# Kernel tuning notes

Hardware: AMD Instinct MI355X
Metric: run time of the kernel (lower is better)

Reference implementation:

```python
import jax, jax.numpy as jnp
import numpy as np
import math

B, S, D, H = 4, 2048, 768, 12
HD = D // H  # 64


def setup_inputs() -> dict:
    key = jax.random.key(0)
    ks = jax.random.split(key, 9)
    s = 0.02
    return {
        "hidden_states": jax.random.normal(ks[0], (B, S, D), jnp.float32),
        "layout_q": jax.random.normal(ks[1], (B, S, D), jnp.float32),
        "layout_k": jax.random.normal(ks[2], (B, S, D), jnp.float32),
        "attention_mask": jnp.zeros((B, 1, 1, S), jnp.float32),
        "Wq": jax.random.normal(ks[3], (D, D), jnp.float32) * s,
        "bq": jnp.zeros((D,), jnp.float32),
        "Wk": jax.random.normal(ks[4], (D, D), jnp.float32) * s,
        "bk": jnp.zeros((D,), jnp.float32),
        "Wv": jax.random.normal(ks[5], (D, D), jnp.float32) * s,
        "bv": jnp.zeros((D,), jnp.float32),
    }


def _split_heads(x):
    # [B,S,D] -> [B,H,S,HD]
    return x.reshape(B, S, H, HD).transpose(0, 2, 1, 3)


def reference(hidden_states, layout_q, layout_k, attention_mask, Wq, bq, Wk, bk, Wv, bv):
    q = _split_heads(hidden_states @ Wq.T + bq)
    k = _split_heads(hidden_states @ Wk.T + bk)
    v = _split_heads(hidden_states @ Wv.T + bv)
    lq = _split_heads(layout_q)
    lk = _split_heads(layout_k)
    scale = 1.0 / math.sqrt(HD)
    # dual-stream scores: content + layout, both [B,H,S,S]
    scores = (jnp.einsum("bhqd,bhkd->bhqk", q, k)
              + jnp.einsum("bhqd,bhkd->bhqk", lq, lk)) * scale
    scores = scores + attention_mask
    probs = jax.nn.softmax(scores, axis=-1)
    ctx = jnp.einsum("bhqk,bhkd->bhqd", probs, v)
    return ctx.transpose(0, 2, 1, 3).reshape(B, S, D)
```

## Files before the change

### kernel.cpp

```cpp
#include <hip/hip_runtime.h>


typedef __attribute__((ext_vector_type(8))) short short8;
typedef __attribute__((ext_vector_type(4))) float floatx4;

#define LOG2E 1.4426950408889634f
#define QSCL 0.18033688011112042f

static constexpr int Sn = 2048, Dn = 768, Hn = 12, BHn = 48;

__device__ __forceinline__ unsigned short f2bf(float f) {
  unsigned u = __float_as_uint(f);
  u += 0x7FFFu + ((u >> 16) & 1u);
  return (unsigned short)(u >> 16);
}

typedef const __attribute__((address_space(1))) unsigned int* gas_t;
typedef __attribute__((address_space(3))) unsigned int* las_t;
__device__ __forceinline__ void async16(const void* g, void* l) {
  __builtin_amdgcn_global_load_lds((gas_t)g, (las_t)l, 16, 0, 0);
}

__global__ void cast_hs_kernel(const float* __restrict__ in, unsigned short* __restrict__ out, int n4) {
  int i = blockIdx.x * 256 + threadIdx.x;
  if (i >= n4) return;
  float4 v = ((const float4*)in)[i];
  ushort4 o = make_ushort4(f2bf(v.x), f2bf(v.y), f2bf(v.z), f2bf(v.w));
  ((ushort4*)out)[i] = o;
}

__global__ void cast_w_kernel(const float* __restrict__ w0, const float* __restrict__ w1,
                              const float* __restrict__ w2, unsigned short* __restrict__ out) {
  int i = blockIdx.x * 256 + threadIdx.x;
  const float* src = (blockIdx.y == 0) ? w0 : (blockIdx.y == 1) ? w1 : w2;
  float4 v = ((const float4*)src)[i];
  ushort4 o = make_ushort4(f2bf(v.x), f2bf(v.y), f2bf(v.z), f2bf(v.w));
  ((ushort4*)(out + (size_t)blockIdx.y * Dn * Dn))[i] = o;
}

__global__ void pack_layout_kernel(const float* __restrict__ lq, const float* __restrict__ lk,
                                   unsigned short* __restrict__ Qc, unsigned short* __restrict__ Kc) {
  int idx = blockIdx.x * 256 + threadIdx.x;
  const float* src = blockIdx.y ? lk : lq;
  unsigned short* dst = blockIdx.y ? Kc : Qc;
  const float sc = blockIdx.y ? 1.0f : QSCL;
  int d8 = idx & 7;
  int tt = idx >> 3;
  int h = tt % Hn;
  int bs = tt / Hn;
  int b = bs >> 11, s = bs & (Sn - 1);
  float4 v0 = ((const float4*)src)[idx * 2];
  float4 v1 = ((const float4*)src)[idx * 2 + 1];
  short8 o;
  o[0] = (short)f2bf(v0.x * sc); o[1] = (short)f2bf(v0.y * sc);
  o[2] = (short)f2bf(v0.z * sc); o[3] = (short)f2bf(v0.w * sc);
  o[4] = (short)f2bf(v1.x * sc); o[5] = (short)f2bf(v1.y * sc);
  o[6] = (short)f2bf(v1.z * sc); o[7] = (short)f2bf(v1.w * sc);
  size_t off = ((size_t)(b * Hn + h) * Sn + s) * 128 + 64 + d8 * 8;
  *(short8*)(dst + off) = o;
}

__global__ __launch_bounds__(256, 3)
void proj_kernel(const unsigned short* __restrict__ X,
                 const unsigned short* __restrict__ Wb,
                 const float* __restrict__ bq, const float* __restrict__ bk, const float* __restrict__ bv,
                 unsigned short* __restrict__ Qc, unsigned short* __restrict__ Kc,
                 unsigned short* __restrict__ Vt) {
  __shared__ __align__(16) unsigned short sMem[16384];
  unsigned short* const sA = sMem;
  unsigned short* const sB = sMem + 8192;

  const int z = blockIdx.z;
  const unsigned short* W = Wb + (size_t)z * Dn * Dn;
  const float* bias = (z == 0) ? bq : (z == 1) ? bk : bv;

  const int t = threadIdx.x;
  const int lane = t & 63, wave = t >> 6;
  const int wm = wave >> 1, wn = wave & 1;
  const int quad = lane >> 4, col15 = lane & 15;
  const int m0 = blockIdx.y * 128, n0 = blockIdx.x * 128;

  const int srow = lane >> 3, schunk = lane & 7;

  floatx4 acc[4][4];
#pragma unroll
  for (int i = 0; i < 4; i++)
#pragma unroll
    for (int j = 0; j < 4; j++) acc[i][j] = (floatx4){0.f, 0.f, 0.f, 0.f};

  for (int k0 = 0; k0 < Dn; k0 += 64) {
    __syncthreads();
#pragma unroll
    for (int c = 0; c < 4; c++) {
      int row = wave * 32 + c * 8 + srow;
      int g = schunk ^ (row & 7);
      async16(X + (size_t)(m0 + row) * Dn + k0 + g * 8, sA + (wave * 32 + c * 8) * 64);
      async16(W + (size_t)(n0 + row) * Dn + k0 + g * 8, sB + (wave * 32 + c * 8) * 64);
    }
    __syncthreads();
#pragma unroll
    for (int kk = 0; kk < 2; kk++) {
      short8 af[4], bf[4];
      const int slot = ((kk * 4 + quad) ^ (col15 & 7)) * 8;
#pragma unroll
      for (int i = 0; i < 4; i++)
        af[i] = *(const short8*)(sA + (wm * 64 + i * 16 + col15) * 64 + slot);
#pragma unroll
      for (int j = 0; j < 4; j++)
        bf[j] = *(const short8*)(sB + (wn * 64 + j * 16 + col15) * 64 + slot);
#pragma unroll
      for (int i = 0; i < 4; i++)
#pragma unroll
        for (int j = 0; j < 4; j++)
          acc[i][j] = __builtin_amdgcn_mfma_f32_16x16x32_bf16(af[i], bf[j], acc[i][j], 0, 0, 0);
    }
  }

  __syncthreads();
  const int b = m0 >> 11;
  const int s0g = m0 & (Sn - 1);
  const int h0 = n0 >> 6;

  if (z < 2) {
    const float scl = (z == 0) ? QSCL : 1.0f;
    unsigned short* dst0 = (z == 0) ? Qc : Kc;
#pragma unroll
    for (int j = 0; j < 4; j++) {
      int nl = wn * 64 + j * 16 + col15;
      float bias_n = bias[n0 + nl];
#pragma unroll
      for (int i = 0; i < 4; i++) {
        int mb = wm * 64 + i * 16 + quad * 4;
#pragma unroll
        for (int r = 0; r < 4; r++) {
          int m = mb + r;
          sMem[m * 128 + (nl ^ (((m >> 2) & 3) << 4))] = f2bf((acc[i][j][r] + bias_n) * scl);
        }
      }
    }
    __syncthreads();
#pragma unroll
    for (int cc = 0; cc < 8; cc++) {
      int idx = cc * 256 + t;
      int m = idx >> 4, piece = idx & 15;
      int h = h0 + (piece >> 3), d8 = piece & 7;
      short8 v = *(const short8*)(sMem + m * 128 + (piece ^ (((m >> 2) & 3) << 1)) * 8);
      *(short8*)(dst0 + ((size_t)(b * Hn + h) * Sn + s0g + m) * 128 + d8 * 8) = v;
    }
  } else {
#pragma unroll
    for (int j = 0; j < 4; j++) {
      int nl = wn * 64 + j * 16 + col15;
      float bias_n = bias[n0 + nl];
#pragma unroll
      for (int i = 0; i < 4; i++) {
        int mb = wm * 64 + i * 16 + quad * 4;
        ushort4 pk = make_ushort4(f2bf(acc[i][j][0] + bias_n), f2bf(acc[i][j][1] + bias_n),
                                  f2bf(acc[i][j][2] + bias_n), f2bf(acc[i][j][3] + bias_n));
        *(ushort4*)(sMem + nl * 128 + (mb ^ ((nl & 7) << 4))) = pk;
      }
    }
    __syncthreads();
#pragma unroll
    for (int cc = 0; cc < 8; cc++) {
      int idx = cc * 256 + t;
      int nl = idx >> 4, piece = idx & 15;
      int h = h0 + (nl >> 6), d = nl & 63;
      short8 v = *(const short8*)(sMem + nl * 128 + (piece ^ ((nl & 7) << 1)) * 8);
      *(short8*)(Vt + ((size_t)(b * Hn + h) * 64 + d) * Sn + s0g + piece * 8) = v;
    }
  }
}

__global__ __launch_bounds__(256, 2)
void attn_kernel(const unsigned short* __restrict__ Qc,
                 const unsigned short* __restrict__ Kc,
                 const unsigned short* __restrict__ Vt,
                 const float* __restrict__ mask,
                 float* __restrict__ out) {
  __shared__ __align__(16) unsigned short sK2[2][64 * 128];
  __shared__ __align__(16) unsigned short sV2[2][64 * 64];
  __shared__ __align__(16) unsigned short sS[128 * 64];

  const int t = threadIdx.x;
  const int lane = t & 63, wave = t >> 6;
  const int quad = lane >> 4, col15 = lane & 15;
  const int swz = (col15 & 7) << 3;

  const int id = blockIdx.x;
  const int slot = id >> 3;
  const int bh = (id & 7) + 8 * (slot >> 4);
  const int q0 = (slot & 15) * 128;
  const int b = bh / Hn, h = bh % Hn;

  short8 aq[2][4];
  const unsigned short* Qbase = Qc + ((size_t)bh * Sn + q0) * 128;
#pragma unroll
  for (int i = 0; i < 2; i++)
#pragma unroll
    for (int kk = 0; kk < 4; kk++)
      aq[i][kk] = *(const short8*)(Qbase + (size_t)(wave * 32 + i * 16 + col15) * 128 + kk * 32 + quad * 8);

  floatx4 O[2][4], lacc[2];
#pragma unroll
  for (int i = 0; i < 2; i++) {
    lacc[i] = (floatx4){0.f, 0.f, 0.f, 0.f};
#pragma unroll
    for (int j = 0; j < 4; j++) O[i][j] = (floatx4){0.f, 0.f, 0.f, 0.f};
  }

  short8 aone;
  {
    short onev = (col15 == 0) ? (short)0x3F80 : (short)0;
#pragma unroll
    for (int e = 0; e < 8; e++) aone[e] = onev;
  }

  const unsigned short* Kbase = Kc + (size_t)bh * Sn * 128;
  const unsigned short* Vbase = Vt + (size_t)bh * 64 * Sn;
  const float* mbase = mask + (size_t)b * Sn;

  const int krow = lane >> 4, kslot = lane & 15;
  const int vrow = lane >> 3, vslot = lane & 7;

  auto stageKV = [&](int tile, int buf) {
    unsigned short* sKn = &sK2[buf][0];
    unsigned short* sVn = &sV2[buf][0];
#pragma unroll
    for (int c = 0; c < 4; c++) {
      int row = wave * 16 + c * 4 + krow;
      int g = (kslot & 8) | ((kslot ^ row) & 7);
      async16(Kbase + (size_t)(tile * 64 + row) * 128 + g * 8, sKn + (wave * 16 + c * 4) * 128);
    }
#pragma unroll
    for (int c = 0; c < 2; c++) {
      int row = wave * 16 + c * 8 + vrow;
      int g = vslot ^ (row & 7);
      async16(Vbase + (size_t)row * Sn + tile * 64 + g * 8, sVn + (wave * 16 + c * 8) * 64);
    }
  };

  constexpr int NT = Sn / 64;
  stageKV(0, 0);
  float mcur = mbase[lane] * LOG2E;
  __syncthreads();

  for (int kt = 0; kt < NT; kt++) {
    const int cur = kt & 1;
    if (kt + 1 < NT) stageKV(kt + 1, cur ^ 1);
    const int tn = (kt + 1 < NT) ? kt + 1 : NT - 1;
    float mnew = mbase[tn * 64 + lane] * LOG2E;
    const bool nomask = __all(mcur == 0.0f);
    const unsigned short* sKcur = &sK2[cur][0];
    const unsigned short* sVcur = &sV2[cur][0];

    floatx4 sacc[4][2];
#pragma unroll
    for (int jm = 0; jm < 4; jm++) {
      sacc[jm][0] = (floatx4){0.f, 0.f, 0.f, 0.f};
      sacc[jm][1] = (floatx4){0.f, 0.f, 0.f, 0.f};
    }
    __builtin_amdgcn_s_setprio(1);
#pragma unroll
    for (int kk = 0; kk < 4; kk++) {
      const int slotK = (((kk * 4 + quad) & 8) | (((kk * 4 + quad) ^ col15) & 7)) * 8;
#pragma unroll
      for (int jm = 0; jm < 4; jm++) {
        short8 ak = *(const short8*)(sKcur + (jm * 16 + col15) * 128 + slotK);
        sacc[jm][0] = __builtin_amdgcn_mfma_f32_16x16x32_bf16(ak, aq[0][kk], sacc[jm][0], 0, 0, 0);
        sacc[jm][1] = __builtin_amdgcn_mfma_f32_16x16x32_bf16(ak, aq[1][kk], sacc[jm][1], 0, 0, 0);
      }
    }
    __builtin_amdgcn_s_setprio(0);

    float mvv[4][4];
    if (!nomask) {
#pragma unroll
      for (int jm = 0; jm < 4; jm++)
#pragma unroll
        for (int r = 0; r < 4; r++) mvv[jm][r] = __shfl(mcur, jm * 16 + quad * 4 + r);
    }

#pragma unroll
    for (int iq = 0; iq < 2; iq++) {
      unsigned short* srow = sS + (wave * 32 + iq * 16 + col15) * 64;
#pragma unroll
      for (int jm = 0; jm < 4; jm++) {
        float p0 = sacc[jm][iq][0], p1 = sacc[jm][iq][1];
        float p2 = sacc[jm][iq][2], p3 = sacc[jm][iq][3];
        if (!nomask) { p0 += mvv[jm][0]; p1 += mvv[jm][1]; p2 += mvv[jm][2]; p3 += mvv[jm][3]; }
        p0 = __builtin_amdgcn_exp2f(p0); p1 = __builtin_amdgcn_exp2f(p1);
        p2 = __builtin_amdgcn_exp2f(p2); p3 = __builtin_amdgcn_exp2f(p3);
        uint2 w;
        w.x = (__float_as_uint(p0) >> 16) | (__float_as_uint(p1) & 0xFFFF0000u);
        w.y = (__float_as_uint(p2) >> 16) | (__float_as_uint(p3) & 0xFFFF0000u);
        *(uint2*)(srow + ((jm * 16 + quad * 4) ^ swz)) = w;
      }
    }

    __builtin_amdgcn_s_setprio(1);
#pragma unroll
    for (int kk = 0; kk < 2; kk++) {
      short8 pb0 = *(const short8*)(sS + (wave * 32 + col15) * 64 + ((kk * 32 + quad * 8) ^ swz));
      short8 pb1 = *(const short8*)(sS + (wave * 32 + 16 + col15) * 64 + ((kk * 32 + quad * 8) ^ swz));
      const int slotV = ((kk * 4 + quad) ^ (col15 & 7)) * 8;
#pragma unroll
      for (int jd = 0; jd < 4; jd++) {
        short8 av = *(const short8*)(sVcur + (jd * 16 + col15) * 64 + slotV);
        O[0][jd] = __builtin_amdgcn_mfma_f32_16x16x32_bf16(av, pb0, O[0][jd], 0, 0, 0);
        O[1][jd] = __builtin_amdgcn_mfma_f32_16x16x32_bf16(av, pb1, O[1][jd], 0, 0, 0);
      }
      lacc[0] = __builtin_amdgcn_mfma_f32_16x16x32_bf16(aone, pb0, lacc[0], 0, 0, 0);
      lacc[1] = __builtin_amdgcn_mfma_f32_16x16x32_bf16(aone, pb1, lacc[1], 0, 0, 0);
    }
    __builtin_amdgcn_s_setprio(0);

    __syncthreads();
    mcur = mnew;
  }

#pragma unroll
  for (int iq = 0; iq < 2; iq++) {
    float inv = 1.0f / __shfl(lacc[iq][0], col15);
    int qrow = q0 + wave * 32 + iq * 16 + col15;
    float* obase = out + ((size_t)b * Sn + qrow) * Dn + h * 64 + quad * 4;
#pragma unroll
    for (int jd = 0; jd < 4; jd++) {
      float4 o4 = make_float4(O[iq][jd][0] * inv, O[iq][jd][1] * inv,
                              O[iq][jd][2] * inv, O[iq][jd][3] * inv);
      *(float4*)(obase + jd * 16) = o4;
    }
  }
}

extern "C" void kernel_launch(void* const* d_in, const int* in_sizes, int n_in,
                              void* d_out, int out_size, void* d_ws, size_t ws_size,
                              hipStream_t stream) {
  const float* hs   = (const float*)d_in[0];
  const float* lq   = (const float*)d_in[1];
  const float* lk   = (const float*)d_in[2];
  const float* mask = (const float*)d_in[3];
  const float* Wq   = (const float*)d_in[4];
  const float* bq   = (const float*)d_in[5];
  const float* Wk   = (const float*)d_in[6];
  const float* bk   = (const float*)d_in[7];
  const float* Wv   = (const float*)d_in[8];
  const float* bv   = (const float*)d_in[9];
  float* out = (float*)d_out;

  char* ws = (char*)d_ws;
  unsigned short* Xbf = (unsigned short*)ws;
  unsigned short* Wbf = (unsigned short*)(ws + 12582912);
  unsigned short* Qc  = (unsigned short*)(ws + 12582912 + 3538944);
  unsigned short* Kc  = Qc + (size_t)BHn * Sn * 128;
  unsigned short* Vt  = Kc + (size_t)BHn * Sn * 128;

  cast_hs_kernel<<<6144, 256, 0, stream>>>(hs, Xbf, 1572864);
  cast_w_kernel<<<dim3(576, 3), 256, 0, stream>>>(Wq, Wk, Wv, Wbf);
  pack_layout_kernel<<<dim3(3072, 2), 256, 0, stream>>>(lq, lk, Qc, Kc);
  proj_kernel<<<dim3(6, 64, 3), 256, 0, stream>>>(Xbf, Wbf, bq, bk, bv, Qc, Kc, Vt);
  attn_kernel<<<768, 256, 0, stream>>>(Qc, Kc, Vt, mask, out);
}
```

Measured before the change: 316.2 us.

## Double-buffer projection GEMM, single-buffer K in attention, compute row sums on VALU

The projection GEMM now stages 32-wide K slices into double-buffered LDS so the next tile loads while the current one runs MFMAs, with one barrier per step instead of two. The attention kernel drops K double-buffering to shrink LDS so occupancy can rise to 3 blocks per CU, and issues the next K/V prefetch after the QK^T MFMAs behind a barrier. Softmax row sums are now accumulated with VALU adds on the bf16-truncated probabilities plus cross-lane shuffles, replacing the extra ones-vector MFMAs. The trade-offs are that the next K tile can no longer load while QK^T runs, and the projection's LDS tiles are unswizzled 32-wide rows that may suffer bank conflicts.

Result: faster. 274.9 us (median of 2 runs) (-13.1%).

```diff
diff --git a/kernel.cpp b/kernel.cpp
--- a/kernel.cpp
+++ b/kernel.cpp
@@ -67,8 +67,6 @@
                  unsigned short* __restrict__ Qc, unsigned short* __restrict__ Kc,
                  unsigned short* __restrict__ Vt) {
   __shared__ __align__(16) unsigned short sMem[16384];
-  unsigned short* const sA = sMem;
-  unsigned short* const sB = sMem + 8192;
 
   const int z = blockIdx.z;
   const unsigned short* W = Wb + (size_t)z * Dn * Dn;
@@ -80,7 +78,7 @@
   const int quad = lane >> 4, col15 = lane & 15;
   const int m0 = blockIdx.y * 128, n0 = blockIdx.x * 128;
 
-  const int srow = lane >> 3, schunk = lane & 7;
+  const int srow = lane >> 2, schunk = lane & 3;
 
   floatx4 acc[4][4];
 #pragma unroll
@@ -88,35 +86,40 @@
 #pragma unroll
     for (int j = 0; j < 4; j++) acc[i][j] = (floatx4){0.f, 0.f, 0.f, 0.f};
 
-  for (int k0 = 0; k0 < Dn; k0 += 64) {
-    __syncthreads();
-#pragma unroll
-    for (int c = 0; c < 4; c++) {
-      int row = wave * 32 + c * 8 + srow;
-      int g = schunk ^ (row & 7);
-      async16(X + (size_t)(m0 + row) * Dn + k0 + g * 8, sA + (wave * 32 + c * 8) * 64);
-      async16(W + (size_t)(n0 + row) * Dn + k0 + g * 8, sB + (wave * 32 + c * 8) * 64);
-    }
-    __syncthreads();
-#pragma unroll
-    for (int kk = 0; kk < 2; kk++) {
-      short8 af[4], bf[4];
-      const int slot = ((kk * 4 + quad) ^ (col15 & 7)) * 8;
-#pragma unroll
-      for (int i = 0; i < 4; i++)
-        af[i] = *(const short8*)(sA + (wm * 64 + i * 16 + col15) * 64 + slot);
+  auto stageAB = [&](int kt, int buf) {
+    unsigned short* sA = sMem + buf * 4096;
+    unsigned short* sB = sMem + 8192 + buf * 4096;
+#pragma unroll
+    for (int c = 0; c < 2; c++) {
+      int row = wave * 32 + c * 16 + srow;
+      async16(X + (size_t)(m0 + row) * Dn + kt * 32 + schunk * 8, sA + (wave * 32 + c * 16) * 32);
+      async16(W + (size_t)(n0 + row) * Dn + kt * 32 + schunk * 8, sB + (wave * 32 + c * 16) * 32);
+    }
+  };
+
+  stageAB(0, 0);
+  __syncthreads();
+
+  for (int kt = 0; kt < 24; kt++) {
+    const int cur = kt & 1;
+    if (kt + 1 < 24) stageAB(kt + 1, cur ^ 1);
+    const unsigned short* sA = sMem + cur * 4096;
+    const unsigned short* sB = sMem + 8192 + cur * 4096;
+    short8 af[4], bf[4];
+#pragma unroll
+    for (int i = 0; i < 4; i++)
+      af[i] = *(const short8*)(sA + (wm * 64 + i * 16 + col15) * 32 + quad * 8);
+#pragma unroll
+    for (int j = 0; j < 4; j++)
+      bf[j] = *(const short8*)(sB + (wn * 64 + j * 16 + col15) * 32 + quad * 8);
+#pragma unroll
+    for (int i = 0; i < 4; i++)
 #pragma unroll
       for (int j = 0; j < 4; j++)
-        bf[j] = *(const short8*)(sB + (wn * 64 + j * 16 + col15) * 64 + slot);
-#pragma unroll
-      for (int i = 0; i < 4; i++)
-#pragma unroll
-        for (int j = 0; j < 4; j++)
-          acc[i][j] = __builtin_amdgcn_mfma_f32_16x16x32_bf16(af[i], bf[j], acc[i][j], 0, 0, 0);
-    }
+        acc[i][j] = __builtin_amdgcn_mfma_f32_16x16x32_bf16(af[i], bf[j], acc[i][j], 0, 0, 0);
+    __syncthreads();
   }
 
-  __syncthreads();
   const int b = m0 >> 11;
   const int s0g = m0 & (Sn - 1);
   const int h0 = n0 >> 6;
@@ -172,13 +175,13 @@
   }
 }
 
-__global__ __launch_bounds__(256, 2)
+__global__ __launch_bounds__(256, 3)
 void attn_kernel(const unsigned short* __restrict__ Qc,
                  const unsigned short* __restrict__ Kc,
                  const unsigned short* __restrict__ Vt,
                  const float* __restrict__ mask,
                  float* __restrict__ out) {
-  __shared__ __align__(16) unsigned short sK2[2][64 * 128];
+  __shared__ __align__(16) unsigned short sK[64 * 128];
   __shared__ __align__(16) unsigned short sV2[2][64 * 64];
   __shared__ __align__(16) unsigned short sS[128 * 64];
 
@@ -201,20 +204,12 @@
     for (int kk = 0; kk < 4; kk++)
       aq[i][kk] = *(const short8*)(Qbase + (size_t)(wave * 32 + i * 16 + col15) * 128 + kk * 32 + quad * 8);
 
-  floatx4 O[2][4], lacc[2];
-#pragma unroll
-  for (int i = 0; i < 2; i++) {
-    lacc[i] = (floatx4){0.f, 0.f, 0.f, 0.f};
+  floatx4 O[2][4];
+  float lsum[2] = {0.f, 0.f};
+#pragma unroll
+  for (int i = 0; i < 2; i++)
 #pragma unroll
     for (int j = 0; j < 4; j++) O[i][j] = (floatx4){0.f, 0.f, 0.f, 0.f};
-  }
-
-  short8 aone;
-  {
-    short onev = (col15 == 0) ? (short)0x3F80 : (short)0;
-#pragma unroll
-    for (int e = 0; e < 8; e++) aone[e] = onev;
-  }
 
   const unsigned short* Kbase = Kc + (size_t)bh * Sn * 128;
   const unsigned short* Vbase = Vt + (size_t)bh * 64 * Sn;
@@ -223,15 +218,16 @@
   const int krow = lane >> 4, kslot = lane & 15;
   const int vrow = lane >> 3, vslot = lane & 7;
 
-  auto stageKV = [&](int tile, int buf) {
-    unsigned short* sKn = &sK2[buf][0];
-    unsigned short* sVn = &sV2[buf][0];
+  auto stageK = [&](int tile) {
 #pragma unroll
     for (int c = 0; c < 4; c++) {
       int row = wave * 16 + c * 4 + krow;
       int g = (kslot & 8) | ((kslot ^ row) & 7);
-      async16(Kbase + (size_t)(tile * 64 + row) * 128 + g * 8, sKn + (wave * 16 + c * 4) * 128);
-    }
+      async16(Kbase + (size_t)(tile * 64 + row) * 128 + g * 8, sK + (wave * 16 + c * 4) * 128);
+    }
+  };
+  auto stageV = [&](int tile, int buf) {
+    unsigned short* sVn = &sV2[buf][0];
 #pragma unroll
     for (int c = 0; c < 2; c++) {
       int row = wave * 16 + c * 8 + vrow;
@@ -241,37 +237,43 @@
   };
 
   constexpr int NT = Sn / 64;
-  stageKV(0, 0);
+  stageK(0);
+  stageV(0, 0);
   float mcur = mbase[lane] * LOG2E;
   __syncthreads();
 
   for (int kt = 0; kt < NT; kt++) {
     const int cur = kt & 1;
-    if (kt + 1 < NT) stageKV(kt + 1, cur ^ 1);
+    const unsigned short* sVcur = &sV2[cur][0];
+
+    floatx4 sacc[4][2];
+#pragma unroll
+    for (int jm = 0; jm < 4; jm++) {
+      sacc[jm][0] = (floatx4){0.f, 0.f, 0.f, 0.f};
+      sacc[jm][1] = (floatx4){0.f, 0.f, 0.f, 0.f};
+    }
+    __builtin_amdgcn_s_setprio(1);
+#pragma unroll
+    for (int kk = 0; kk < 4; kk++) {
+      const int slotK = (((kk * 4 + quad) & 8) | (((kk * 4 + quad) ^ col15) & 7)) * 8;
+#pragma unroll
+      for (int jm = 0; jm < 4; jm++) {
+        short8 ak = *(const short8*)(sK + (jm * 16 + col15) * 128 + slotK);
+        sacc[jm][0] = __builtin_amdgcn_mfma_f32_16x16x32_bf16(ak, aq[0][kk], sacc[jm][0], 0, 0, 0);
+        sacc[jm][1] = __builtin_amdgcn_mfma_f32_16x16x32_bf16(ak, aq[1][kk], sacc[jm][1], 0, 0, 0);
+      }
+    }
+    __builtin_amdgcn_s_setprio(0);
+
     const int tn = (kt + 1 < NT) ? kt + 1 : NT - 1;
     float mnew = mbase[tn * 64 + lane] * LOG2E;
     const bool nomask = __all(mcur == 0.0f);
-    const unsigned short* sKcur = &sK2[cur][0];
-    const unsigned short* sVcur = &sV2[cur][0];
-
-    floatx4 sacc[4][2];
-#pragma unroll
-    for (int jm = 0; jm < 4; jm++) {
-      sacc[jm][0] = (floatx4){0.f, 0.f, 0.f, 0.f};
-      sacc[jm][1] = (floatx4){0.f, 0.f, 0.f, 0.f};
-    }
-    __builtin_amdgcn_s_setprio(1);
-#pragma unroll
-    for (int kk = 0; kk < 4; kk++) {
-      const int slotK = (((kk * 4 + quad) & 8) | (((kk * 4 + quad) ^ col15) & 7)) * 8;
-#pragma unroll
-      for (int jm = 0; jm < 4; jm++) {
-        short8 ak = *(const short8*)(sKcur + (jm * 16 + col15) * 128 + slotK);
-        sacc[jm][0] = __builtin_amdgcn_mfma_f32_16x16x32_bf16(ak, aq[0][kk], sacc[jm][0], 0, 0, 0);
-        sacc[jm][1] = __builtin_amdgcn_mfma_f32_16x16x32_bf16(ak, aq[1][kk], sacc[jm][1], 0, 0, 0);
-      }
-    }
-    __builtin_amdgcn_s_setprio(0);
+
+    __syncthreads();
+    if (kt + 1 < NT) {
+      stageK(kt + 1);
+      stageV(kt + 1, cur ^ 1);
+    }
 
     float mvv[4][4];
     if (!nomask) {
@@ -284,18 +286,24 @@
 #pragma unroll
     for (int iq = 0; iq < 2; iq++) {
       unsigned short* srow = sS + (wave * 32 + iq * 16 + col15) * 64;
+      float lacc = 0.f;
 #pragma unroll
       for (int jm = 0; jm < 4; jm++) {
         float p0 = sacc[jm][iq][0], p1 = sacc[jm][iq][1];
         float p2 = sacc[jm][iq][2], p3 = sacc[jm][iq][3];
         if (!nomask) { p0 += mvv[jm][0]; p1 += mvv[jm][1]; p2 += mvv[jm][2]; p3 += mvv[jm][3]; }
-        p0 = __builtin_amdgcn_exp2f(p0); p1 = __builtin_amdgcn_exp2f(p1);
-        p2 = __builtin_amdgcn_exp2f(p2); p3 = __builtin_amdgcn_exp2f(p3);
+        unsigned u0 = __float_as_uint(__builtin_amdgcn_exp2f(p0)) & 0xFFFF0000u;
+        unsigned u1 = __float_as_uint(__builtin_amdgcn_exp2f(p1)) & 0xFFFF0000u;
+        unsigned u2 = __float_as_uint(__builtin_amdgcn_exp2f(p2)) & 0xFFFF0000u;
+        unsigned u3 = __float_as_uint(__builtin_amdgcn_exp2f(p3)) & 0xFFFF0000u;
+        lacc += (__uint_as_float(u0) + __uint_as_float(u1)) +
+                (__uint_as_float(u2) + __uint_as_float(u3));
         uint2 w;
-        w.x = (__float_as_uint(p0) >> 16) | (__float_as_uint(p1) & 0xFFFF0000u);
-        w.y = (__float_as_uint(p2) >> 16) | (__float_as_uint(p3) & 0xFFFF0000u);
+        w.x = (u0 >> 16) | u1;
+        w.y = (u2 >> 16) | u3;
         *(uint2*)(srow + ((jm * 16 + quad * 4) ^ swz)) = w;
       }
+      lsum[iq] += lacc;
     }
 
     __builtin_amdgcn_s_setprio(1);
@@ -310,8 +318,6 @@
         O[0][jd] = __builtin_amdgcn_mfma_f32_16x16x32_bf16(av, pb0, O[0][jd], 0, 0, 0);
         O[1][jd] = __builtin_amdgcn_mfma_f32_16x16x32_bf16(av, pb1, O[1][jd], 0, 0, 0);
       }
-      lacc[0] = __builtin_amdgcn_mfma_f32_16x16x32_bf16(aone, pb0, lacc[0], 0, 0, 0);
-      lacc[1] = __builtin_amdgcn_mfma_f32_16x16x32_bf16(aone, pb1, lacc[1], 0, 0, 0);
     }
     __builtin_amdgcn_s_setprio(0);
 
@@ -321,7 +327,10 @@
 
 #pragma unroll
   for (int iq = 0; iq < 2; iq++) {
-    float inv = 1.0f / __shfl(lacc[iq][0], col15);
+    float s_ = lsum[iq];
+    s_ += __shfl_xor(s_, 16);
+    s_ += __shfl_xor(s_, 32);
+    float inv = 1.0f / s_;
     int qrow = q0 + wave * 32 + iq * 16 + col15;
     float* obase = out + ((size_t)b * Sn + qrow) * Dn + h * 64 + quad * 4;
 #pragma unroll
```
